# Performance work log

Hardware: AMD Instinct MI355X
Metric: run time of the kernel (lower is better)

## Reference

```python
import jax, jax.numpy as jnp
import numpy as np


def setup_inputs() -> dict:
    key = jax.random.key(0)
    k1, k2 = jax.random.split(key)
    B, C, H, W = 16, 256, 64, 64
    K, D = 1024, 256
    z = jax.random.normal(k1, (B, C, H, W), dtype=jnp.float32)
    embedding = jax.random.normal(k2, (K, D), dtype=jnp.float32)
    return {"z": z, "embedding": embedding}


def reference(z, embedding):
    # _preprocess: shift channel dim (axis 1) to last, flatten -> [N, D]
    B, C, H, W = z.shape
    encoded_permuted = jnp.transpose(z, (0, 2, 3, 1))  # [B, H, W, C]
    permuted_shape = encoded_permuted.shape
    encoded_flat = encoded_permuted.reshape(-1, C)  # [N, D]

    x_sq = jnp.sum(encoded_flat * encoded_flat, axis=1, keepdims=True)  # [N, 1]
    e_sq = jnp.sum(embedding * embedding, axis=1)  # [K]
    cross = encoded_flat @ embedding.T  # [N, K]
    distances = x_sq - 2.0 * cross + e_sq[None, :]
    codebook_indices = jnp.argmin(distances, axis=1)  # [N]
    quantized_lookup = embedding[codebook_indices]  # [N, D]

    # straight-through estimator
    quantized_flat = encoded_flat + jax.lax.stop_gradient(quantized_lookup - encoded_flat)

    # _postprocess: reshape and shift last dim back to axis 1
    quantized = jnp.transpose(quantized_flat.reshape(permuted_shape), (0, 3, 1, 2))
    return (encoded_flat, quantized_flat, codebook_indices, quantized)
```

## Files before the change

### kernel.cpp

```cpp
#include <hip/hip_runtime.h>
#include <hip/hip_bf16.h>

typedef _Float16 h8 __attribute__((ext_vector_type(8)));
typedef float f4 __attribute__((ext_vector_type(4)));

#define N_TOK 65536
#define DIM 256
#define KCODES 1024
#define HWSZ 4096

__device__ __forceinline__ void gll16(const void* g, void* l) {
    __builtin_amdgcn_global_load_lds((const __attribute__((address_space(1))) void*)g,
                                     (__attribute__((address_space(3))) void*)l, 16, 0, 0);
}


__global__ void k_prep_frag(const float* __restrict__ emb, _Float16* __restrict__ BhF,
                            _Float16* __restrict__ BlF) {
    int gi = blockIdx.x * 256 + threadIdx.x;
    int kb = gi >> 9;
    int s = (gi >> 6) & 7;
    int dq = (gi >> 4) & 3;
    int r = gi & 15;
    int code = kb * 16 + r;
    int d0 = s * 32 + dq * 8;
    const float* src = emb + (size_t)code * DIM + d0;
    float4 x0 = *(const float4*)(src);
    float4 x1 = *(const float4*)(src + 4);
    float xs[8] = {x0.x, x0.y, x0.z, x0.w, x1.x, x1.y, x1.z, x1.w};
    h8 hi, lo;
#pragma unroll
    for (int j = 0; j < 8; ++j) {
        _Float16 h = (_Float16)xs[j];
        hi[j] = h;
        lo[j] = (_Float16)(xs[j] - (float)h);
    }
    *(h8*)(BhF + (size_t)gi * 8) = hi;
    *(h8*)(BlF + (size_t)gi * 8) = lo;
}

__global__ void k_esq(const float* __restrict__ emb, float* __restrict__ e_sq) {
    int t = threadIdx.x;
    int code = blockIdx.x * 4 + (t >> 6);
    int l = t & 63;
    float4 v = *(const float4*)(emb + (size_t)code * DIM + l * 4);
    float s = v.x * v.x + v.y * v.y + v.z * v.z + v.w * v.w;
#pragma unroll
    for (int off = 32; off >= 1; off >>= 1) s += __shfl_xor(s, off);
    if (l == 0) e_sq[code] = s;
}

__global__ void k_transpose(const float* __restrict__ z, float* __restrict__ enc,
                            _Float16* __restrict__ AhF, _Float16* __restrict__ AlF) {
    __shared__ float T[64][65];
    int blk = blockIdx.x;
    int b = blk >> 8;
    int rem = blk & 255;
    int c0 = (rem >> 6) * 64;
    int hw0 = (rem & 63) * 64;
    int t = threadIdx.x;
    const float* zp = z + (size_t)b * DIM * HWSZ;
    {
        int hw4 = (t & 15) * 4, cl = t >> 4;
#pragma unroll
        for (int i = 0; i < 4; ++i) {
            int c = cl + i * 16;
            float4 v = *(const float4*)(zp + (size_t)(c0 + c) * HWSZ + hw0 + hw4);
            T[c][hw4 + 0] = v.x; T[c][hw4 + 1] = v.y;
            T[c][hw4 + 2] = v.z; T[c][hw4 + 3] = v.w;
        }
    }
    __syncthreads();
    {
        int c4 = (t & 15) * 4, hwl = t >> 4;
#pragma unroll
        for (int i = 0; i < 4; ++i) {
            int hw = hwl + i * 16;
            float4 v;
            v.x = T[c4 + 0][hw]; v.y = T[c4 + 1][hw];
            v.z = T[c4 + 2][hw]; v.w = T[c4 + 3][hw];
            *(float4*)(enc + (size_t)(b * HWSZ + hw0 + hw) * DIM + c0 + c4) = v;
        }
    }
    {
        int base_nb = b * 256 + (hw0 >> 4);
#pragma unroll
        for (int i = 0; i < 2; ++i) {
            int gidx = i * 256 + t;
            int nbi = gidx >> 7;
            int si = (gidx >> 6) & 1;
            int dq = (gidx >> 4) & 3;
            int r = gidx & 15;
            int hwl = nbi * 16 + r;
            int cl = si * 32 + dq * 8;
            h8 hi, lo;
#pragma unroll
            for (int j = 0; j < 8; ++j) {
                float x = T[cl + j][hwl];
                _Float16 h = (_Float16)x;
                hi[j] = h;
                lo[j] = (_Float16)(x - (float)h);
            }
            size_t G = (((size_t)(base_nb + nbi) * 8) + (c0 >> 5) + si) * 64 + dq * 16 + r;
            *(h8*)(AhF + G * 8) = hi;
            *(h8*)(AlF + G * 8) = lo;
        }
    }
}

#define WAITV(n) asm volatile("s_waitcnt vmcnt(" #n ")" ::: "memory")
#define BARRIER __builtin_amdgcn_s_barrier()
#define PRIO1 __builtin_amdgcn_s_setprio(1)
#define PRIO0 __builtin_amdgcn_s_setprio(0)

extern __shared__ char SB[];

__global__ __launch_bounds__(1024)
void k_gemm_argmin(const _Float16* __restrict__ AhF, const _Float16* __restrict__ AlF,
                   const _Float16* __restrict__ BhF, const _Float16* __restrict__ BlF,
                   const float* __restrict__ e_sq,
                   float* __restrict__ pV1, int* __restrict__ pI1) {
    int gid = blockIdx.x;
    int rchunk = gid >> 8;
    int colTile = (gid >> 6) & 3;
    int rowTile = rchunk * 64 + (gid & 63);
    int r0 = rowTile * 128, c0 = colTile * 256;
    int t = threadIdx.x;
    int w = t >> 6, l = t & 63;
    int wm = w >> 2, wn = w & 3;
    int l16 = l & 15, lhi = l >> 4;

    const char* gAh = (const char*)AhF + (((size_t)(rowTile * 8 + w)) << 13) + (l << 4);
    const char* gAl = (const char*)AlF + (((size_t)(rowTile * 8 + w)) << 13) + (l << 4);
    const char* gBh0 = (const char*)BhF + (((size_t)(colTile * 16 + 2 * w)) << 13) + (l << 4);
    const char* gBh1 = gBh0 + (1ll << 13);
    const char* gBl0 = (const char*)BlF + (((size_t)(colTile * 16 + 2 * w)) << 13) + (l << 4);
    const char* gBl1 = gBl0 + (1ll << 13);

#define ISSUE_P(p) do { \
    const int s_ = (p) >> 1, buf_ = (p) % 6; \
    const char* a_ = ((p) & 1) ? gAl : gAh; \
    const char* b0_ = ((p) & 1) ? gBl0 : gBh0; \
    const char* b1_ = ((p) & 1) ? gBl1 : gBh1; \
    char* bp_ = SB + buf_ * 24576; \
    gll16(a_ + (s_ << 10), bp_ + (w << 10)); \
    gll16(b0_ + (s_ << 10), bp_ + 8192 + ((2 * w) << 10)); \
    gll16(b1_ + (s_ << 10), bp_ + 8192 + ((2 * w + 1) << 10)); \
} while (0)

#define READ_A(buf, dst) { const char* bp_ = SB + (buf) * 24576; \
    _Pragma("unroll") for (int mf = 0; mf < 2; ++mf) \
        dst[mf] = *(const h8*)(bp_ + ((wm * 2 + mf) << 10) + (l << 4)); }
#define READ_B(buf, dst) { const char* bp_ = SB + (buf) * 24576 + 8192; \
    _Pragma("unroll") for (int nf = 0; nf < 4; ++nf) \
        dst[nf] = *(const h8*)(bp_ + ((wn * 4 + nf) << 10) + (l << 4)); }
#define MFMA8(A_, B_) { _Pragma("unroll") for (int mf = 0; mf < 2; ++mf) \
    _Pragma("unroll") for (int nf = 0; nf < 4; ++nf) \
        acc[mf][nf] = __builtin_amdgcn_mfma_f32_16x16x32_f16(A_[mf], B_[nf], acc[mf][nf], 0, 0, 0); }

#define PHASE(q, W, DO_ISSUE) \
    if (w < 8) { WAITV(W); } \
    BARRIER; \
    if ((DO_ISSUE) && w < 8) { ISSUE_P((q) + 5); } \
    if (((q) & 1) == 0) { \
        READ_A((q) % 6, ah); READ_B((q) % 6, bh); \
        PRIO1; MFMA8(ah, bh); PRIO0; \
    } else { \
        READ_A((q) % 6, al); READ_B((q) % 6, bl); \
        PRIO1; MFMA8(ah, bl); MFMA8(al, bh); PRIO0; \
    }

    f4 acc[2][4];
#pragma unroll
    for (int i = 0; i < 2; ++i)
#pragma unroll
        for (int j = 0; j < 4; ++j) acc[i][j] = (f4)0.0f;

    h8 ah[2], al[2], bh[4], bl[4];

    if (w < 8) { ISSUE_P(0); ISSUE_P(1); ISSUE_P(2); ISSUE_P(3); ISSUE_P(4); }

    PHASE(0, 12, 1)  PHASE(1, 12, 1)  PHASE(2, 12, 1)  PHASE(3, 12, 1)
    PHASE(4, 12, 1)  PHASE(5, 12, 1)  PHASE(6, 12, 1)  PHASE(7, 12, 1)
    PHASE(8, 12, 1)  PHASE(9, 12, 1)  PHASE(10, 12, 1) PHASE(11, 12, 0)
    PHASE(12, 9, 0)  PHASE(13, 6, 0)  PHASE(14, 3, 0)  PHASE(15, 0, 0)

    float* smV = (float*)SB;
    int* smI = (int*)(SB + 2048);

    float esq[4];
#pragma unroll
    for (int nf = 0; nf < 4; ++nf) esq[nf] = e_sq[c0 + wn * 64 + nf * 16 + l16];

#pragma unroll
    for (int mf = 0; mf < 2; ++mf) {
#pragma unroll
        for (int rg = 0; rg < 4; ++rg) {
            float bestV = 3.4e38f;
            int bestI = 0;
#pragma unroll
            for (int nf = 0; nf < 4; ++nf) {
                float v = esq[nf] - 2.0f * acc[mf][nf][rg];
                int ci = c0 + wn * 64 + nf * 16 + l16;
                if (v < bestV || (v == bestV && ci < bestI)) { bestV = v; bestI = ci; }
            }
#pragma unroll
            for (int off = 1; off < 16; off <<= 1) {
                float vv = __shfl_xor(bestV, off);
                int ii = __shfl_xor(bestI, off);
                if (vv < bestV || (vv == bestV && ii < bestI)) { bestV = vv; bestI = ii; }
            }
            if (l16 == 0) {
                int rloc = wm * 32 + mf * 16 + lhi * 4 + rg;
                smV[wn * 128 + rloc] = bestV;
                smI[wn * 128 + rloc] = bestI;
            }
        }
    }
    __syncthreads();
    if (t < 128) {
        float bestV = smV[t];
        int bestI = smI[t];
#pragma unroll
        for (int wn2 = 1; wn2 < 4; ++wn2) {
            float v = smV[wn2 * 128 + t];
            int i2 = smI[wn2 * 128 + t];
            if (v < bestV || (v == bestV && i2 < bestI)) { bestV = v; bestI = i2; }
        }
        pV1[colTile * N_TOK + r0 + t] = bestV;
        pI1[colTile * N_TOK + r0 + t] = bestI;
    }
}

__global__ void k_final_out1(const float* __restrict__ pV1, const int* __restrict__ pI1,
                             const float* __restrict__ emb,
                             float* __restrict__ out2, int* __restrict__ idxI,
                             float* __restrict__ out1) {
    __shared__ int sidx[256];
    int t = threadIdx.x;
    int n0 = blockIdx.x * 256;
    int n = n0 + t;
    float v1 = pV1[n];
    int i1 = pI1[n];
#pragma unroll
    for (int ct = 1; ct < 4; ++ct) {
        float a1 = pV1[ct * N_TOK + n];
        int ai = pI1[ct * N_TOK + n];
        if (a1 < v1 || (a1 == v1 && ai < i1)) { v1 = a1; i1 = ai; }
    }
    out2[n] = (float)i1;
    idxI[n] = i1;
    sidx[t] = i1;
    __syncthreads();
    int rr = t >> 2, q = t & 3;
#pragma unroll
    for (int i = 0; i < 4; ++i) {
        int r = i * 64 + rr;
        int idx = sidx[r];
        const float* src = emb + (size_t)idx * DIM + q * 64;
        float* dst = out1 + (size_t)(n0 + r) * DIM + q * 64;
#pragma unroll
        for (int j = 0; j < 16; ++j)
            *(float4*)(dst + j * 4) = *(const float4*)(src + j * 4);
    }
}

__global__ void k_out3(const float* __restrict__ emb, const int* __restrict__ idxI,
                       float* __restrict__ out3) {
    __shared__ float E[32][257];
    int blk = blockIdx.x;
    int b = blk >> 7, hwt = blk & 127;
    int hw0 = hwt * 32;
    int n0 = b * HWSZ + hw0;
    int t = threadIdx.x;
    {
        int r = t >> 3, oct = t & 7;
        int idx = idxI[n0 + r];
        const float* src = emb + (size_t)idx * DIM + oct * 32;
#pragma unroll
        for (int i = 0; i < 8; ++i) {
            float4 v = *(const float4*)(src + i * 4);
            E[r][oct * 32 + i * 4 + 0] = v.x;
            E[r][oct * 32 + i * 4 + 1] = v.y;
            E[r][oct * 32 + i * 4 + 2] = v.z;
            E[r][oct * 32 + i * 4 + 3] = v.w;
        }
    }
    __syncthreads();
    {
        int w = t >> 6, l = t & 63;
        int ch = l >> 5, hw = l & 31;
        float* dst = out3 + (size_t)b * DIM * HWSZ + hw0 + hw;
#pragma unroll
        for (int it = 0; it < 32; ++it) {
            int c = w * 64 + it * 2 + ch;
            dst[(size_t)c * HWSZ] = E[hw][c];
        }
    }
}

extern "C" void kernel_launch(void* const* d_in, const int* in_sizes, int n_in,
                              void* d_out, int out_size, void* d_ws, size_t ws_size,
                              hipStream_t stream) {
    const float* z = (const float*)d_in[0];
    const float* emb = (const float*)d_in[1];
    float* out = (float*)d_out;
    float* out0 = out;
    float* out1 = out + 16777216;
    float* out2 = out + 33554432;
    float* out3 = out + 33619968;

    _Float16* AhF = (_Float16*)out1;
    _Float16* AlF = (_Float16*)(out1 + 8388608);

    char* ws = (char*)d_ws;
    _Float16* BhF = (_Float16*)(ws);
    _Float16* BlF = (_Float16*)(ws + 524288);
    float* e_sq = (float*)(ws + 1048576);
    float* pV1 = (float*)(ws + 1052672);
    int* pI1 = (int*)(ws + 2101248);
    int* idxI = (int*)(ws + 3149824);

    static bool attr_set = false;
    if (!attr_set) {
        hipFuncSetAttribute((const void*)k_gemm_argmin,
                            hipFuncAttributeMaxDynamicSharedMemorySize, 147456);
        attr_set = true;
    }

    k_prep_frag<<<128, 256, 0, stream>>>(emb, BhF, BlF);
    k_esq<<<256, 256, 0, stream>>>(emb, e_sq);
    k_transpose<<<4096, 256, 0, stream>>>(z, out0, AhF, AlF);
    k_gemm_argmin<<<2048, 1024, 147456, stream>>>(AhF, AlF, BhF, BlF, e_sq, pV1, pI1);
    k_final_out1<<<256, 256, 0, stream>>>(pV1, pI1, emb, out2, idxI, out1);
    k_out3<<<2048, 256, 0, stream>>>(emb, idxI, out3);
}
```

Measured before the change: 209.9 us.

## Enlarge GEMM-argmin block tile to 256x256 with four-deep LDS ring

The fused distance GEMM plus argmin kernel moves from 128x256 to 256x256 output tiles per block. Each warp now computes a 64x64 sub-tile (4x4 MFMA fragments), and each of the 16 warps issues one A and one B load per stage. The six-slot LDS ring becomes a four-slot ring of 32 KB with prefetch distance three, and the low-part fragments are read just in time to save registers. The aim is more arithmetic per byte loaded and fewer blocks, at the cost of higher register pressure and a shallower prefetch pipeline.

```diff
diff --git a/kernel.cpp b/kernel.cpp
--- a/kernel.cpp
+++ b/kernel.cpp
@@ -121,79 +121,77 @@
                    const float* __restrict__ e_sq,
                    float* __restrict__ pV1, int* __restrict__ pI1) {
     int gid = blockIdx.x;
-    int rchunk = gid >> 8;
-    int colTile = (gid >> 6) & 3;
-    int rowTile = rchunk * 64 + (gid & 63);
-    int r0 = rowTile * 128, c0 = colTile * 256;
+    int colTile = gid >> 8;
+    int rowTile = gid & 255;
+    int r0 = rowTile * 256, c0 = colTile * 256;
     int t = threadIdx.x;
     int w = t >> 6, l = t & 63;
     int wm = w >> 2, wn = w & 3;
     int l16 = l & 15, lhi = l >> 4;
 
-    const char* gAh = (const char*)AhF + (((size_t)(rowTile * 8 + w)) << 13) + (l << 4);
-    const char* gAl = (const char*)AlF + (((size_t)(rowTile * 8 + w)) << 13) + (l << 4);
-    const char* gBh0 = (const char*)BhF + (((size_t)(colTile * 16 + 2 * w)) << 13) + (l << 4);
-    const char* gBh1 = gBh0 + (1ll << 13);
-    const char* gBl0 = (const char*)BlF + (((size_t)(colTile * 16 + 2 * w)) << 13) + (l << 4);
-    const char* gBl1 = gBl0 + (1ll << 13);
+    const char* gAh = (const char*)AhF + (((size_t)(rowTile * 16 + w)) << 13) + (l << 4);
+    const char* gAl = (const char*)AlF + (((size_t)(rowTile * 16 + w)) << 13) + (l << 4);
+    const char* gBh = (const char*)BhF + (((size_t)(colTile * 16 + w)) << 13) + (l << 4);
+    const char* gBl = (const char*)BlF + (((size_t)(colTile * 16 + w)) << 13) + (l << 4);
 
 #define ISSUE_P(p) do { \
-    const int s_ = (p) >> 1, buf_ = (p) % 6; \
+    const int s_ = (p) >> 1; \
+    char* bp_ = SB + ((p) & 3) * 32768; \
     const char* a_ = ((p) & 1) ? gAl : gAh; \
-    const char* b0_ = ((p) & 1) ? gBl0 : gBh0; \
-    const char* b1_ = ((p) & 1) ? gBl1 : gBh1; \
-    char* bp_ = SB + buf_ * 24576; \
+    const char* b_ = ((p) & 1) ? gBl : gBh; \
     gll16(a_ + (s_ << 10), bp_ + (w << 10)); \
-    gll16(b0_ + (s_ << 10), bp_ + 8192 + ((2 * w) << 10)); \
-    gll16(b1_ + (s_ << 10), bp_ + 8192 + ((2 * w + 1) << 10)); \
+    gll16(b_ + (s_ << 10), bp_ + 16384 + (w << 10)); \
 } while (0)
 
-#define READ_A(buf, dst) { const char* bp_ = SB + (buf) * 24576; \
-    _Pragma("unroll") for (int mf = 0; mf < 2; ++mf) \
-        dst[mf] = *(const h8*)(bp_ + ((wm * 2 + mf) << 10) + (l << 4)); }
-#define READ_B(buf, dst) { const char* bp_ = SB + (buf) * 24576 + 8192; \
-    _Pragma("unroll") for (int nf = 0; nf < 4; ++nf) \
-        dst[nf] = *(const h8*)(bp_ + ((wn * 4 + nf) << 10) + (l << 4)); }
-#define MFMA8(A_, B_) { _Pragma("unroll") for (int mf = 0; mf < 2; ++mf) \
+#define MFMA16(A_, B_) { _Pragma("unroll") for (int mf = 0; mf < 4; ++mf) \
     _Pragma("unroll") for (int nf = 0; nf < 4; ++nf) \
         acc[mf][nf] = __builtin_amdgcn_mfma_f32_16x16x32_f16(A_[mf], B_[nf], acc[mf][nf], 0, 0, 0); }
 
-#define PHASE(q, W, DO_ISSUE) \
-    if (w < 8) { WAITV(W); } \
+#define PHASE(q, W, DO_ISSUE) { \
+    WAITV(W); \
     BARRIER; \
-    if ((DO_ISSUE) && w < 8) { ISSUE_P((q) + 5); } \
+    if (DO_ISSUE) ISSUE_P((q) + 3); \
+    const char* bp_ = SB + ((q) & 3) * 32768; \
     if (((q) & 1) == 0) { \
-        READ_A((q) % 6, ah); READ_B((q) % 6, bh); \
-        PRIO1; MFMA8(ah, bh); PRIO0; \
+        _Pragma("unroll") for (int mf = 0; mf < 4; ++mf) \
+            ah[mf] = *(const h8*)(bp_ + ((wm * 4 + mf) << 10) + (l << 4)); \
+        _Pragma("unroll") for (int nf = 0; nf < 4; ++nf) \
+            bh[nf] = *(const h8*)(bp_ + 16384 + ((wn * 4 + nf) << 10) + (l << 4)); \
+        PRIO1; MFMA16(ah, bh); PRIO0; \
     } else { \
-        READ_A((q) % 6, al); READ_B((q) % 6, bl); \
-        PRIO1; MFMA8(ah, bl); MFMA8(al, bh); PRIO0; \
-    }
-
-    f4 acc[2][4];
-#pragma unroll
-    for (int i = 0; i < 2; ++i)
+        h8 xl[4]; \
+        _Pragma("unroll") for (int nf = 0; nf < 4; ++nf) \
+            xl[nf] = *(const h8*)(bp_ + 16384 + ((wn * 4 + nf) << 10) + (l << 4)); \
+        PRIO1; MFMA16(ah, xl); PRIO0; \
+        _Pragma("unroll") for (int mf = 0; mf < 4; ++mf) \
+            xl[mf] = *(const h8*)(bp_ + ((wm * 4 + mf) << 10) + (l << 4)); \
+        PRIO1; MFMA16(xl, bh); PRIO0; \
+    } }
+
+    f4 acc[4][4];
+#pragma unroll
+    for (int i = 0; i < 4; ++i)
 #pragma unroll
         for (int j = 0; j < 4; ++j) acc[i][j] = (f4)0.0f;
 
-    h8 ah[2], al[2], bh[4], bl[4];
-
-    if (w < 8) { ISSUE_P(0); ISSUE_P(1); ISSUE_P(2); ISSUE_P(3); ISSUE_P(4); }
-
-    PHASE(0, 12, 1)  PHASE(1, 12, 1)  PHASE(2, 12, 1)  PHASE(3, 12, 1)
-    PHASE(4, 12, 1)  PHASE(5, 12, 1)  PHASE(6, 12, 1)  PHASE(7, 12, 1)
-    PHASE(8, 12, 1)  PHASE(9, 12, 1)  PHASE(10, 12, 1) PHASE(11, 12, 0)
-    PHASE(12, 9, 0)  PHASE(13, 6, 0)  PHASE(14, 3, 0)  PHASE(15, 0, 0)
+    h8 ah[4], bh[4];
+
+    ISSUE_P(0); ISSUE_P(1); ISSUE_P(2);
+
+    PHASE(0, 4, 1)   PHASE(1, 4, 1)   PHASE(2, 4, 1)   PHASE(3, 4, 1)
+    PHASE(4, 4, 1)   PHASE(5, 4, 1)   PHASE(6, 4, 1)   PHASE(7, 4, 1)
+    PHASE(8, 4, 1)   PHASE(9, 4, 1)   PHASE(10, 4, 1)  PHASE(11, 4, 1)
+    PHASE(12, 4, 1)  PHASE(13, 4, 0)  PHASE(14, 2, 0)  PHASE(15, 0, 0)
 
     float* smV = (float*)SB;
-    int* smI = (int*)(SB + 2048);
+    int* smI = (int*)(SB + 4096);
 
     float esq[4];
 #pragma unroll
     for (int nf = 0; nf < 4; ++nf) esq[nf] = e_sq[c0 + wn * 64 + nf * 16 + l16];
 
 #pragma unroll
-    for (int mf = 0; mf < 2; ++mf) {
+    for (int mf = 0; mf < 4; ++mf) {
 #pragma unroll
         for (int rg = 0; rg < 4; ++rg) {
             float bestV = 3.4e38f;
@@ -211,20 +209,20 @@
                 if (vv < bestV || (vv == bestV && ii < bestI)) { bestV = vv; bestI = ii; }
             }
             if (l16 == 0) {
-                int rloc = wm * 32 + mf * 16 + lhi * 4 + rg;
-                smV[wn * 128 + rloc] = bestV;
-                smI[wn * 128 + rloc] = bestI;
+                int rloc = wm * 64 + mf * 16 + lhi * 4 + rg;
+                smV[wn * 256 + rloc] = bestV;
+                smI[wn * 256 + rloc] = bestI;
             }
         }
     }
     __syncthreads();
-    if (t < 128) {
+    if (t < 256) {
         float bestV = smV[t];
         int bestI = smI[t];
 #pragma unroll
         for (int wn2 = 1; wn2 < 4; ++wn2) {
-            float v = smV[wn2 * 128 + t];
-            int i2 = smI[wn2 * 128 + t];
+            float v = smV[wn2 * 256 + t];
+            int i2 = smI[wn2 * 256 + t];
             if (v < bestV || (v == bestV && i2 < bestI)) { bestV = v; bestI = i2; }
         }
         pV1[colTile * N_TOK + r0 + t] = bestV;
@@ -324,14 +322,14 @@
     static bool attr_set = false;
     if (!attr_set) {
         hipFuncSetAttribute((const void*)k_gemm_argmin,
-                            hipFuncAttributeMaxDynamicSharedMemorySize, 147456);
+                            hipFuncAttributeMaxDynamicSharedMemorySize, 131072);
         attr_set = true;
     }
 
     k_prep_frag<<<128, 256, 0, stream>>>(emb, BhF, BlF);
     k_esq<<<256, 256, 0, stream>>>(emb, e_sq);
     k_transpose<<<4096, 256, 0, stream>>>(z, out0, AhF, AlF);
-    k_gemm_argmin<<<2048, 1024, 147456, stream>>>(AhF, AlF, BhF, BlF, e_sq, pV1, pI1);
+    k_gemm_argmin<<<1024, 1024, 131072, stream>>>(AhF, AlF, BhF, BlF, e_sq, pV1, pI1);
     k_final_out1<<<256, 256, 0, stream>>>(pV1, pI1, emb, out2, idxI, out1);
     k_out3<<<2048, 256, 0, stream>>>(emb, idxI, out3);
 }
```

New measurement: 222.4 us. 6.0% more time.
